# Kernel optimization log

Measured on AMD Instinct MI355X. Metric: run time of the kernel, lower is better.

The kernel has to match this reference:

```python
import jax, jax.numpy as jnp
import numpy as np

K = 7  # kernel_size


def setup_inputs() -> dict:
    key = jax.random.key(0)
    k1, k2 = jax.random.split(key)
    kernels = jax.random.normal(k1, (4, K, K, 256, 256), dtype=jnp.float32)
    features = jax.random.normal(k2, (4, 96, 256, 256), dtype=jnp.float32)
    return {"kernels": kernels, "features": features}


def reference(kernels, features):
    # kernels: [b, k, k, h, w]; features: [b, c, h, w]
    # Equivalent to unfold(features) viewed as [b,c,k,k,h,w] contracted with
    # kernels via einsum 'bcklhw,bklhw->bchw', but computed as a fused sum of
    # k*k shifted products to avoid materializing the k^2-larger intermediate.
    b, c, h, w = features.shape
    k = kernels.shape[1]
    p = k // 2
    fpad = jnp.pad(features, ((0, 0), (0, 0), (p, p), (p, p)))
    out = jnp.zeros_like(features)
    for i in range(k):  # small fixed loop over kernel taps (k*k = 49)
        for j in range(k):
            out = out + fpad[:, :, i:i + h, j:j + w] * kernels[:, i, j][:, None]
    return out
```

## Files before the change

### kernel.cpp

```cpp
#include <hip/hip_runtime.h>


#define BATCH 4
#define CHAN 96
#define HW_ 256
#define HWPIX 65536
#define KS 7
#define XT 64
#define YT 16
#define NTHR 512
#define XPITCH 72
#define ROWSTRIDE (CHAN * XPITCH)
#define RING_S (8 * ROWSTRIDE)
#define NPAIR 36
#define FSLOTS (CHAN * NPAIR)
#define FSPT 7
#define BT_K 24
#define BT_NROW (KS * BT_K)
#define BT_STRIP (16 * BT_NROW)
#define BT_BUF (4 * BT_STRIP)
#define KVALS (KS * KS * XT)
#define KSPT 7
#define LDS_BYTES ((RING_S + 2 * BT_BUF) * 2)

typedef __attribute__((ext_vector_type(8))) short short8v;
typedef __attribute__((ext_vector_type(4))) float f32x4;

static __device__ __forceinline__ unsigned short f2bf(float x) {
    union { float f; unsigned u; } v; v.f = x;
    unsigned u = v.u + 0x7fffu + ((v.u >> 16) & 1u);
    return (unsigned short)(u >> 16);
}

__global__ __launch_bounds__(NTHR)
void svconv_mfma2(const float* __restrict__ K_, const float* __restrict__ F_,
                  float* __restrict__ O_) {
    extern __shared__ short lds[];
    unsigned* lds32 = (unsigned*)lds;
    short* BT = lds + RING_S;

    const int tid = threadIdx.x;
    const int xt = blockIdx.x, yt = blockIdx.y, b = blockIdx.z;
    const int gx0 = xt * XT, gy0 = yt * YT;
    const int wave = tid >> 6, lane = tid & 63;
    const int nt = wave & 3, ch = wave >> 2;
    const int n = lane & 15, kb = lane >> 4;

    {
        unsigned* bt32 = (unsigned*)BT;
#pragma unroll
        for (int i = 0; i < BT_BUF / NTHR; ++i)
            bt32[tid + NTHR * i] = 0u;
    }

    int fldsoff[FSPT], fgof[FSPT];
    bool fm0[FSPT], fm1[FSPT];
#pragma unroll
    for (int i = 0; i < FSPT; ++i) {
        int idx = tid + NTHR * i;
        if (idx < FSLOTS) {
            int c = idx / NPAIR;
            int xi0 = 2 * (idx - c * NPAIR);
            int x0e = gx0 - 3 + xi0;
            fldsoff[i] = c * XPITCH + xi0;
            fgof[i] = c * HWPIX + x0e;
            fm0[i] = ((unsigned)x0e < (unsigned)HW_);
            fm1[i] = ((unsigned)(x0e + 1) < (unsigned)HW_);
        } else { fldsoff[i] = -1; fgof[i] = 0; fm0[i] = false; fm1[i] = false; }
    }

    int kgoff[KSPT], kldsoff[KSPT];
#pragma unroll
    for (int i = 0; i < KSPT; ++i) {
        int idx = tid + NTHR * i;
        if (idx < KVALS) {
            int dydx = idx >> 6, xl = idx & 63;
            int dy = dydx / KS, dx = dydx - KS * dy;
            int sn = xl & 15, snt = xl >> 4;
            kgoff[i] = dydx * HWPIX + gx0 + xl;
            kldsoff[i] = snt * BT_STRIP + sn * BT_NROW + dy * BT_K + (sn + dx);
        } else { kgoff[i] = 0; kldsoff[i] = -1; }
    }

    const float* Fb = F_ + (size_t)b * CHAN * HWPIX;
    const float* Kb = K_ + (size_t)b * KS * KS * HWPIX;

    __syncthreads();

    for (int r = -3; r <= 3; ++r) {
        int yr = gy0 + r;
        bool yok = ((unsigned)yr < (unsigned)HW_);
        int rbase = (yr & 7) * ROWSTRIDE;
#pragma unroll
        for (int i = 0; i < FSPT; ++i) {
            if (fldsoff[i] >= 0) {
                float f0 = 0.f, f1 = 0.f;
                if (yok && fm0[i]) f0 = Fb[(size_t)yr * HW_ + fgof[i]];
                if (yok && fm1[i]) f1 = Fb[(size_t)yr * HW_ + fgof[i] + 1];
                lds32[(rbase + fldsoff[i]) >> 1] =
                    (unsigned)f2bf(f0) | ((unsigned)f2bf(f1) << 16);
            }
        }
    }
#pragma unroll
    for (int i = 0; i < KSPT; ++i)
        if (kldsoff[i] >= 0)
            BT[kldsoff[i]] = (short)f2bf(Kb[kgoff[i] + gy0 * HW_]);

    float rr0[FSPT], rr1[FSPT], krf[KSPT];
    {
        const int yr = gy0 + 4;
#pragma unroll
        for (int i = 0; i < FSPT; ++i) {
            rr0[i] = 0.f; rr1[i] = 0.f;
            if (fm0[i]) rr0[i] = Fb[(size_t)yr * HW_ + fgof[i]];
            if (fm1[i]) rr1[i] = Fb[(size_t)yr * HW_ + fgof[i] + 1];
        }
#pragma unroll
        for (int i = 0; i < KSPT; ++i)
            krf[i] = (kldsoff[i] >= 0) ? Kb[kgoff[i] + (gy0 + 1) * HW_] : 0.f;
    }

    const int kcl8 = (kb == 3) ? 0 : kb * 8;
    const int aoffc = (ch * 48 + n) * XPITCH + nt * 16 + kcl8;
    float* ob = O_ + ((size_t)(b * CHAN + ch * 48 + kb * 4)) * HWPIX
              + gx0 + nt * 16 + n;
    const short8v bzero = {0, 0, 0, 0, 0, 0, 0, 0};

#pragma unroll 1
    for (int t = 0; t < YT; ++t) {
        const int y = gy0 + t;
        __syncthreads();

        const short* btp = BT + (t & 1) * BT_BUF + nt * BT_STRIP + n * BT_NROW + kb * 8;
        short8v bfr[KS];
#pragma unroll
        for (int dy = 0; dy < KS; ++dy)
            bfr[dy] = (kb < 3) ? *(const short8v*)(btp + dy * BT_K) : bzero;

        f32x4 acc0 = {0,0,0,0}, acc1 = {0,0,0,0}, acc2 = {0,0,0,0};
#pragma unroll
        for (int dy = 0; dy < KS; ++dy) {
            const short* ap = lds + ((y + dy - 3) & 7) * ROWSTRIDE + aoffc;
            acc0 = __builtin_amdgcn_mfma_f32_16x16x32_bf16(*(const short8v*)(ap), bfr[dy], acc0, 0, 0, 0);
            acc1 = __builtin_amdgcn_mfma_f32_16x16x32_bf16(*(const short8v*)(ap + 16 * XPITCH), bfr[dy], acc1, 0, 0, 0);
            acc2 = __builtin_amdgcn_mfma_f32_16x16x32_bf16(*(const short8v*)(ap + 32 * XPITCH), bfr[dy], acc2, 0, 0, 0);
        }

        {
            float* op = ob + (size_t)y * HW_;
#pragma unroll
            for (int r = 0; r < 4; ++r) {
                op[(size_t)r * HWPIX]        = acc0[r];
                op[(size_t)(16 + r) * HWPIX] = acc1[r];
                op[(size_t)(32 + r) * HWPIX] = acc2[r];
            }
        }

        if (t < YT - 1) {
            int rbase = ((y + 4) & 7) * ROWSTRIDE;
#pragma unroll
            for (int i = 0; i < FSPT; ++i)
                if (fldsoff[i] >= 0)
                    lds32[(rbase + fldsoff[i]) >> 1] =
                        (unsigned)f2bf(rr0[i]) | ((unsigned)f2bf(rr1[i]) << 16);
            short* btw = BT + ((t + 1) & 1) * BT_BUF;
#pragma unroll
            for (int i = 0; i < KSPT; ++i)
                if (kldsoff[i] >= 0) btw[kldsoff[i]] = (short)f2bf(krf[i]);
        }

        if (t < YT - 2) {
            int yr = y + 5;
            bool yok = ((unsigned)yr < (unsigned)HW_);
#pragma unroll
            for (int i = 0; i < FSPT; ++i) {
                rr0[i] = 0.f; rr1[i] = 0.f;
                if (yok && fm0[i]) rr0[i] = Fb[(size_t)yr * HW_ + fgof[i]];
                if (yok && fm1[i]) rr1[i] = Fb[(size_t)yr * HW_ + fgof[i] + 1];
            }
            const int yk = y + 2;
#pragma unroll
            for (int i = 0; i < KSPT; ++i)
                if (kldsoff[i] >= 0) krf[i] = Kb[kgoff[i] + yk * HW_];
        }
    }
}

extern "C" void kernel_launch(void* const* d_in, const int* in_sizes, int n_in,
                              void* d_out, int out_size, void* d_ws, size_t ws_size,
                              hipStream_t stream) {
    const float* kernels  = (const float*)d_in[0];
    const float* features = (const float*)d_in[1];
    float* out = (float*)d_out;

    hipFuncSetAttribute(reinterpret_cast<const void*>(&svconv_mfma2),
                        hipFuncAttributeMaxDynamicSharedMemorySize, LDS_BYTES);

    dim3 grid(HW_ / XT, HW_ / YT, BATCH);
    dim3 block(NTHR);
    svconv_mfma2<<<grid, block, LDS_BYTES, stream>>>(kernels, features, out);
}
```

Before: 74.74 us.

## Load feature MFMA operands directly into a register ring instead of an LDS ring

Removes the LDS ring buffer for feature rows. Each lane now loads its own 8-wide bf16 A-fragment straight from global memory with float4 loads into an 8-slot register ring, and the time loop is fully unrolled so the ring slots stay static. This cuts LDS traffic and the large dynamic LDS allocation, which may raise occupancy. In exchange it adds register pressure (24 short8v plus prefetch buffers) and redundant global loads across waves. Bf16 conversion now uses HIP intrinsics, and the kernel-weight strip layout is padded and offset by one.

```diff
diff --git a/kernel.cpp b/kernel.cpp
--- a/kernel.cpp
+++ b/kernel.cpp
@@ -1,4 +1,5 @@
 #include <hip/hip_runtime.h>
+#include <hip/hip_bf16.h>
 
 
 #define BATCH 4
@@ -9,35 +10,36 @@
 #define XT 64
 #define YT 16
 #define NTHR 512
-#define XPITCH 72
-#define ROWSTRIDE (CHAN * XPITCH)
-#define RING_S (8 * ROWSTRIDE)
-#define NPAIR 36
-#define FSLOTS (CHAN * NPAIR)
-#define FSPT 7
 #define BT_K 24
 #define BT_NROW (KS * BT_K)
-#define BT_STRIP (16 * BT_NROW)
+#define BT_STRIP (16 * BT_NROW + 8)
 #define BT_BUF (4 * BT_STRIP)
 #define KVALS (KS * KS * XT)
 #define KSPT 7
-#define LDS_BYTES ((RING_S + 2 * BT_BUF) * 2)
+#define FTOT ((size_t)BATCH * CHAN * HWPIX)
 
 typedef __attribute__((ext_vector_type(8))) short short8v;
 typedef __attribute__((ext_vector_type(4))) float f32x4;
 
-static __device__ __forceinline__ unsigned short f2bf(float x) {
-    union { float f; unsigned u; } v; v.f = x;
-    unsigned u = v.u + 0x7fffu + ((v.u >> 16) & 1u);
-    return (unsigned short)(u >> 16);
-}
+union S8 { short8v s; unsigned u[4]; };
+
+static __device__ __forceinline__ unsigned pkbf(float a, float b) {
+    union { __hip_bfloat162 h; unsigned u; } c;
+    c.h = __float22bfloat162_rn(make_float2(a, b));
+    return c.u;
+}
+static __device__ __forceinline__ short bfbits(float x) {
+    union { __hip_bfloat16 h; short s; } c;
+    c.h = __float2bfloat16(x);
+    return c.s;
+}
+
+struct AF { float4 v[3][2]; };
 
 __global__ __launch_bounds__(NTHR)
-void svconv_mfma2(const float* __restrict__ K_, const float* __restrict__ F_,
+void svconv_mfma4(const float* __restrict__ K_, const float* __restrict__ F_,
                   float* __restrict__ O_) {
-    extern __shared__ short lds[];
-    unsigned* lds32 = (unsigned*)lds;
-    short* BT = lds + RING_S;
+    __shared__ short BT[2 * BT_BUF];
 
     const int tid = threadIdx.x;
     const int xt = blockIdx.x, yt = blockIdx.y, b = blockIdx.z;
@@ -46,28 +48,51 @@
     const int nt = wave & 3, ch = wave >> 2;
     const int n = lane & 15, kb = lane >> 4;
 
-    {
-        unsigned* bt32 = (unsigned*)BT;
-#pragma unroll
-        for (int i = 0; i < BT_BUF / NTHR; ++i)
-            bt32[tid + NTHR * i] = 0u;
-    }
-
-    int fldsoff[FSPT], fgof[FSPT];
-    bool fm0[FSPT], fm1[FSPT];
-#pragma unroll
-    for (int i = 0; i < FSPT; ++i) {
-        int idx = tid + NTHR * i;
-        if (idx < FSLOTS) {
-            int c = idx / NPAIR;
-            int xi0 = 2 * (idx - c * NPAIR);
-            int x0e = gx0 - 3 + xi0;
-            fldsoff[i] = c * XPITCH + xi0;
-            fgof[i] = c * HWPIX + x0e;
-            fm0[i] = ((unsigned)x0e < (unsigned)HW_);
-            fm1[i] = ((unsigned)(x0e + 1) < (unsigned)HW_);
-        } else { fldsoff[i] = -1; fgof[i] = 0; fm0[i] = false; fm1[i] = false; }
-    }
+    const int xs = gx0 - 4 + nt * 16 + kb * 8;
+    const float* lo = F_;
+    const float* hiq = F_ + FTOT - 4;
+    const float* abase[3];
+#pragma unroll
+    for (int ct = 0; ct < 3; ++ct)
+        abase[ct] = F_ + ((size_t)(b * CHAN + ch * 48 + ct * 16 + n)) * HWPIX + xs;
+
+    unsigned xm[4];
+#pragma unroll
+    for (int i = 0; i < 4; ++i) {
+        unsigned m0 = ((unsigned)(xs + 2 * i) < (unsigned)HW_) ? 0xFFFFu : 0u;
+        unsigned m1 = ((unsigned)(xs + 2 * i + 1) < (unsigned)HW_) ? 0xFFFFu : 0u;
+        xm[i] = m0 | (m1 << 16);
+    }
+
+    short8v ar[8][3];
+
+    auto issueA = [&](int yr, AF& f) {
+#pragma unroll
+        for (int ct = 0; ct < 3; ++ct) {
+            const float* p = abase[ct] + (size_t)yr * HW_;
+            const float* p0 = p;
+            const float* p1 = p + 4;
+            p0 = p0 < lo ? lo : (p0 > hiq ? hiq : p0);
+            p1 = p1 < lo ? lo : (p1 > hiq ? hiq : p1);
+            f.v[ct][0] = *(const float4*)p0;
+            f.v[ct][1] = *(const float4*)p1;
+        }
+    };
+    auto commitA = [&](int slot, const AF& f, bool yok) {
+#pragma unroll
+        for (int ct = 0; ct < 3; ++ct) {
+            S8 v;
+            if (yok) {
+                v.u[0] = pkbf(f.v[ct][0].x, f.v[ct][0].y) & xm[0];
+                v.u[1] = pkbf(f.v[ct][0].z, f.v[ct][0].w) & xm[1];
+                v.u[2] = pkbf(f.v[ct][1].x, f.v[ct][1].y) & xm[2];
+                v.u[3] = pkbf(f.v[ct][1].z, f.v[ct][1].w) & xm[3];
+            } else {
+                v.u[0] = 0; v.u[1] = 0; v.u[2] = 0; v.u[3] = 0;
+            }
+            ar[slot][ct] = v.s;
+        }
+    };
 
     int kgoff[KSPT], kldsoff[KSPT];
 #pragma unroll
@@ -78,60 +103,62 @@
             int dy = dydx / KS, dx = dydx - KS * dy;
             int sn = xl & 15, snt = xl >> 4;
             kgoff[i] = dydx * HWPIX + gx0 + xl;
-            kldsoff[i] = snt * BT_STRIP + sn * BT_NROW + dy * BT_K + (sn + dx);
+            kldsoff[i] = snt * BT_STRIP + sn * BT_NROW + dy * BT_K + (sn + dx + 1);
         } else { kgoff[i] = 0; kldsoff[i] = -1; }
     }
-
-    const float* Fb = F_ + (size_t)b * CHAN * HWPIX;
     const float* Kb = K_ + (size_t)b * KS * KS * HWPIX;
 
+    {
+        unsigned* bt32 = (unsigned*)BT;
+#pragma unroll
+        for (int i = 0; i < 22; ++i) {
+            int idx = tid + NTHR * i;
+            if (idx < BT_BUF) bt32[idx] = 0u;
+        }
+    }
+
+    float kr0[KSPT];
+#pragma unroll
+    for (int i = 0; i < KSPT; ++i)
+        kr0[i] = (kldsoff[i] >= 0) ? Kb[kgoff[i] + (size_t)gy0 * HW_] : 0.f;
+
     __syncthreads();
 
-    for (int r = -3; r <= 3; ++r) {
-        int yr = gy0 + r;
-        bool yok = ((unsigned)yr < (unsigned)HW_);
-        int rbase = (yr & 7) * ROWSTRIDE;
-#pragma unroll
-        for (int i = 0; i < FSPT; ++i) {
-            if (fldsoff[i] >= 0) {
-                float f0 = 0.f, f1 = 0.f;
-                if (yok && fm0[i]) f0 = Fb[(size_t)yr * HW_ + fgof[i]];
-                if (yok && fm1[i]) f1 = Fb[(size_t)yr * HW_ + fgof[i] + 1];
-                lds32[(rbase + fldsoff[i]) >> 1] =
-                    (unsigned)f2bf(f0) | ((unsigned)f2bf(f1) << 16);
-            }
-        }
-    }
+    AF afa, afb;
+    issueA(gy0 - 3, afa);
+#pragma unroll
+    for (int r = 0; r < 7; ++r) {
+        AF& cur = (r & 1) ? afb : afa;
+        AF& nxt = (r & 1) ? afa : afb;
+        if (r < 6) issueA(gy0 + r - 2, nxt);
+        const int yr = gy0 + r - 3;
+        commitA((r + 5) & 7, cur, (unsigned)yr < (unsigned)HW_);
+    }
+
 #pragma unroll
     for (int i = 0; i < KSPT; ++i)
-        if (kldsoff[i] >= 0)
-            BT[kldsoff[i]] = (short)f2bf(Kb[kgoff[i] + gy0 * HW_]);
-
-    float rr0[FSPT], rr1[FSPT], krf[KSPT];
-    {
-        const int yr = gy0 + 4;
-#pragma unroll
-        for (int i = 0; i < FSPT; ++i) {
-            rr0[i] = 0.f; rr1[i] = 0.f;
-            if (fm0[i]) rr0[i] = Fb[(size_t)yr * HW_ + fgof[i]];
-            if (fm1[i]) rr1[i] = Fb[(size_t)yr * HW_ + fgof[i] + 1];
-        }
-#pragma unroll
-        for (int i = 0; i < KSPT; ++i)
-            krf[i] = (kldsoff[i] >= 0) ? Kb[kgoff[i] + (gy0 + 1) * HW_] : 0.f;
-    }
-
-    const int kcl8 = (kb == 3) ? 0 : kb * 8;
-    const int aoffc = (ch * 48 + n) * XPITCH + nt * 16 + kcl8;
+        if (kldsoff[i] >= 0) BT[kldsoff[i]] = bfbits(kr0[i]);
+
+    const short8v bzero = {0, 0, 0, 0, 0, 0, 0, 0};
     float* ob = O_ + ((size_t)(b * CHAN + ch * 48 + kb * 4)) * HWPIX
               + gx0 + nt * 16 + n;
-    const short8v bzero = {0, 0, 0, 0, 0, 0, 0, 0};
-
-#pragma unroll 1
+    float krf[KSPT];
+    AF af;
+
+#pragma unroll
     for (int t = 0; t < YT; ++t) {
         const int y = gy0 + t;
         __syncthreads();
 
+        if (t < YT - 1) {
+#pragma unroll
+            for (int i = 0; i < KSPT; ++i)
+                krf[i] = (kldsoff[i] >= 0)
+                       ? Kb[kgoff[i] + (size_t)(y + 1) * HW_] : 0.f;
+        }
+        const bool pyok = (y + 4 < HW_);
+        if (pyok) issueA(y + 4, af);
+
         const short* btp = BT + (t & 1) * BT_BUF + nt * BT_STRIP + n * BT_NROW + kb * 8;
         short8v bfr[KS];
 #pragma unroll
@@ -141,10 +168,10 @@
         f32x4 acc0 = {0,0,0,0}, acc1 = {0,0,0,0}, acc2 = {0,0,0,0};
 #pragma unroll
         for (int dy = 0; dy < KS; ++dy) {
-            const short* ap = lds + ((y + dy - 3) & 7) * ROWSTRIDE + aoffc;
-            acc0 = __builtin_amdgcn_mfma_f32_16x16x32_bf16(*(const short8v*)(ap), bfr[dy], acc0, 0, 0, 0);
-            acc1 = __builtin_amdgcn_mfma_f32_16x16x32_bf16(*(const short8v*)(ap + 16 * XPITCH), bfr[dy], acc1, 0, 0, 0);
-            acc2 = __builtin_amdgcn_mfma_f32_16x16x32_bf16(*(const short8v*)(ap + 32 * XPITCH), bfr[dy], acc2, 0, 0, 0);
+            const int sl = (t + dy + 5) & 7;
+            acc0 = __builtin_amdgcn_mfma_f32_16x16x32_bf16(ar[sl][0], bfr[dy], acc0, 0, 0, 0);
+            acc1 = __builtin_amdgcn_mfma_f32_16x16x32_bf16(ar[sl][1], bfr[dy], acc1, 0, 0, 0);
+            acc2 = __builtin_amdgcn_mfma_f32_16x16x32_bf16(ar[sl][2], bfr[dy], acc2, 0, 0, 0);
         }
 
         {
@@ -157,32 +184,13 @@
             }
         }
 
+        commitA((t + 4) & 7, af, pyok);
+
         if (t < YT - 1) {
-            int rbase = ((y + 4) & 7) * ROWSTRIDE;
-#pragma unroll
-            for (int i = 0; i < FSPT; ++i)
-                if (fldsoff[i] >= 0)
-                    lds32[(rbase + fldsoff[i]) >> 1] =
-                        (unsigned)f2bf(rr0[i]) | ((unsigned)f2bf(rr1[i]) << 16);
             short* btw = BT + ((t + 1) & 1) * BT_BUF;
 #pragma unroll
             for (int i = 0; i < KSPT; ++i)
-                if (kldsoff[i] >= 0) btw[kldsoff[i]] = (short)f2bf(krf[i]);
-        }
-
-        if (t < YT - 2) {
-            int yr = y + 5;
-            bool yok = ((unsigned)yr < (unsigned)HW_);
-#pragma unroll
-            for (int i = 0; i < FSPT; ++i) {
-                rr0[i] = 0.f; rr1[i] = 0.f;
-                if (yok && fm0[i]) rr0[i] = Fb[(size_t)yr * HW_ + fgof[i]];
-                if (yok && fm1[i]) rr1[i] = Fb[(size_t)yr * HW_ + fgof[i] + 1];
-            }
-            const int yk = y + 2;
-#pragma unroll
-            for (int i = 0; i < KSPT; ++i)
-                if (kldsoff[i] >= 0) krf[i] = Kb[kgoff[i] + yk * HW_];
+                if (kldsoff[i] >= 0) btw[kldsoff[i]] = bfbits(krf[i]);
         }
     }
 }
@@ -194,10 +202,7 @@
     const float* features = (const float*)d_in[1];
     float* out = (float*)d_out;
 
-    hipFuncSetAttribute(reinterpret_cast<const void*>(&svconv_mfma2),
-                        hipFuncAttributeMaxDynamicSharedMemorySize, LDS_BYTES);
-
     dim3 grid(HW_ / XT, HW_ / YT, BATCH);
     dim3 block(NTHR);
-    svconv_mfma2<<<grid, block, LDS_BYTES, stream>>>(kernels, features, out);
-}
+    svconv_mfma4<<<grid, block, 0, stream>>>(kernels, features, out);
+}
```

Result: slower. 83.91 us (+12.3%).
